# Performance work log

Hardware: AMD Instinct MI355X
Metric: run time of the kernel (lower is better)

## Reference

```python
import jax, jax.numpy as jnp
import numpy as np

N, D, W, S = 16384, 256, 64, 8  # utterances, embed dim, attention half-window, speakers


def setup_inputs() -> dict:
    key = jax.random.key(0)
    ks = jax.random.split(key, 8)
    scale = 1.0 / np.sqrt(D)
    return {
        "x": jax.random.normal(ks[0], (N, D), jnp.float32),
        "speaker_ids": jax.random.randint(ks[1], (N,), 0, S, jnp.int32),
        "W_att": jax.random.normal(ks[2], (D, D), jnp.float32) * scale,
        "W_pred": jax.random.normal(ks[3], (D, D), jnp.float32) * scale,
        "W_suc": jax.random.normal(ks[4], (D, D), jnp.float32) * scale,
        "W_same": jax.random.normal(ks[5], (D, D), jnp.float32) * scale,
        "W_diff": jax.random.normal(ks[6], (D, D), jnp.float32) * scale,
    }


def reference(x, speaker_ids, W_att, W_pred, W_suc, W_same, W_diff):
    n = x.shape[0]
    pad = jnp.zeros((W, D), x.dtype)
    # windowed gather: for utterance i, neighbors at offsets [-W, W-1] (2W slots)
    win_idx = jnp.arange(n)[:, None] + jnp.arange(2 * W)[None, :]  # index into padded [N+2W]
    xp = jnp.concatenate([pad, x, pad], axis=0)                    # [N+2W, D]
    windows = xp[win_idx]                                          # [N, 2W, D]
    # raw_attn[i,w] = (edge_att_weights(windows[i,w])) . x[i]
    raw_attn = jnp.einsum("nwd,ed,ne->nw", windows, W_att, x)      # [N, 2W]
    attn = jax.nn.softmax(raw_attn, axis=1)
    # relation masks over the band: j = i + offset
    offs = jnp.arange(2 * W) - W                                   # [-W, W-1]
    j = jnp.arange(n)[:, None] + offs[None, :]                     # [N, 2W]
    valid = (j >= 0) & (j < n)
    jc = jnp.clip(j, 0, n - 1)
    same_spk = speaker_ids[jc] == speaker_ids[:, None]
    masks = [
        valid & (offs >= 0)[None, :],   # pred: edges to current/future within window
        valid & (offs < 0)[None, :],    # suc: edges to past within window
        valid & same_spk,               # same speaker within window
        valid & ~same_spk,              # different speaker within window
    ]
    # relation-specific GCN aggregation: h = sum_r A_r @ (x @ W_r), A_r banded
    h = jnp.zeros_like(x)
    for Wr, m in zip([W_pred, W_suc, W_same, W_diff], masks):
        support = x @ Wr                                           # [N, D]
        sp = jnp.concatenate([pad, support, pad], axis=0)[win_idx]  # [N, 2W, D]
        h = h + jnp.einsum("nw,nwd->nd", attn * m, sp)
    return jax.nn.log_softmax(h, axis=1)
```

## Files before the change

### kernel.cpp

```cpp
#include <hip/hip_runtime.h>
#include <hip/hip_bf16.h>

typedef unsigned short u16;
typedef unsigned int u32;
typedef __attribute__((ext_vector_type(8))) short short8;
typedef __attribute__((ext_vector_type(4))) float floatx4;

#define NU 16384
#define DIM 256
#define AMS 200
#define AC1o 12800u
#define YLO 16896u
#define STGo 33792u

#define XHo 0u
#define XLo 4194304u
#define ST0 20971520u
#define STROW 16512u
#define STMAT 4227072u
#define WH0o 33652736u
#define WL0o 33718272u
#define WRo  33783808u

__device__ __forceinline__ u16 bfh(float v) {
  return (u16)(__float_as_uint(v) >> 16);
}
__device__ __forceinline__ float bup(u16 u) {
  return __uint_as_float(((u32)u) << 16);
}
__device__ __forceinline__ u16 bfrn(float v) {
  u32 u = __float_as_uint(v);
  return (u16)((u + 0x7fffu + ((u >> 16) & 1u)) >> 16);
}

__device__ __forceinline__ void gload16(const u16* g, u16* l) {
  __builtin_amdgcn_global_load_lds(
      (__attribute__((address_space(1))) void*)(uintptr_t)g,
      (__attribute__((address_space(3))) void*)(uintptr_t)l, 16, 0, 0);
}

__global__ __launch_bounds__(256) void prep(
    const float* __restrict__ x,
    const float* __restrict__ wat, const float* __restrict__ wpr,
    const float* __restrict__ wsu, const float* __restrict__ wsm,
    const float* __restrict__ wdf, u16* __restrict__ ws) {
  const int b = blockIdx.x, t = threadIdx.x;
  if (b < 2048) {
    int idx = (b * 256 + t) * 8;
    float4 v0 = *(const float4*)(x + idx);
    float4 v1 = *(const float4*)(x + idx + 4);
    float a[8] = {v0.x, v0.y, v0.z, v0.w, v1.x, v1.y, v1.z, v1.w};
    u16 h[8], l[8];
#pragma unroll
    for (int q = 0; q < 8; ++q) {
      h[q] = bfh(a[q]);
      l[q] = bfh(a[q] - bup(h[q]));
    }
    *(uint4*)(ws + XHo + idx) = *(const uint4*)h;
    *(uint4*)(ws + XLo + idx) = *(const uint4*)l;
    return;
  }
  const int b2 = b - 2048;
  if (b2 < 32) {
    const int s = b2 & 7, mat = b2 >> 3, n = t;
    const float* Wa = (mat == 0) ? wat : (mat == 1) ? wpr : (mat == 2) ? wsm : wsu;
    const float* Wb = (mat == 0) ? wat : (mat == 1) ? wsu : (mat == 2) ? wdf : wdf;
    const float c1  = (mat == 0) ? 0.f : (mat == 3) ? 1.f : -1.f;
    u16 hbuf[32], lbuf[32];
#pragma unroll 8
    for (int k = 0; k < 32; ++k) {
      float v = Wa[(s * 32 + k) * 256 + n] + c1 * Wb[(s * 32 + k) * 256 + n];
      if (mat == 0) { hbuf[k] = bfh(v); lbuf[k] = bfh(v - bup(hbuf[k])); }
      else          { hbuf[k] = bfrn(v); }
    }
    u16* dh = ws + ((mat == 0) ? WH0o : (WRo + (size_t)(mat - 1) * 65536))
               + (size_t)s * 8192 + n * 32;
#pragma unroll
    for (int p = 0; p < 4; ++p) *(uint4*)(dh + p * 8) = ((const uint4*)hbuf)[p];
    if (mat == 0) {
      u16* dl = ws + WL0o + (size_t)s * 8192 + n * 32;
#pragma unroll
      for (int p = 0; p < 4; ++p) *(uint4*)(dl + p * 8) = ((const uint4*)lbuf)[p];
    }
  } else {
    int g = (b2 - 32) * 256 + t;
    int r = g >> 13, rem = g & 8191;
    int d = rem >> 5, p = rem & 31;
    size_t base = ST0 + (size_t)r * STMAT + (size_t)d * STROW;
    size_t off = (p < 16) ? (base + p * 4) : (base + 16448 + (p - 16) * 4);
    *(ushort4*)(ws + off) = make_ushort4(0, 0, 0, 0);
  }
}

__global__ __launch_bounds__(512, 4) void gemmS1(const float* __restrict__ x,
                                                 u16* __restrict__ ws) {
  __shared__ __align__(16) u16 U[39168];

  const int t = threadIdx.x, row0 = blockIdx.x * 32;
  const int w = t >> 6, ln = t & 15, quad = (t & 63) >> 4, q8 = quad * 8;
  const int n0 = w * 32;

#pragma unroll
  for (int cc = 0; cc < 4; ++cc) {
    int idx = t + 512 * cc;
    int row = idx >> 6, c4 = (idx & 63) * 4;
    float4 v = *(const float4*)(x + (size_t)(row0 + row) * 256 + c4);
    ushort4 pk = make_ushort4(bfrn(v.x), bfrn(v.y), bfrn(v.z), bfrn(v.w));
    *(ushort4*)(U + row * 264 + c4) = pk;
  }
  __syncthreads();

  floatx4 acc[3][2][2];
#pragma unroll
  for (int mat = 0; mat < 3; ++mat)
#pragma unroll
    for (int m = 0; m < 2; ++m)
#pragma unroll
      for (int nt = 0; nt < 2; ++nt) acc[mat][m][nt] = (floatx4){0.f, 0.f, 0.f, 0.f};

  for (int s = 0; s < 8; ++s) {
    short8 ah[2];
#pragma unroll
    for (int m = 0; m < 2; ++m)
      ah[m] = *(const short8*)(U + (m * 16 + ln) * 264 + s * 32 + q8);
#pragma unroll
    for (int mat = 0; mat < 3; ++mat) {
      short8 bh[2];
#pragma unroll
      for (int nt = 0; nt < 2; ++nt)
        bh[nt] = *(const short8*)(ws + WRo + (size_t)mat * 65536
                                  + (size_t)s * 8192 + (n0 + nt * 16 + ln) * 32 + q8);
#pragma unroll
      for (int m = 0; m < 2; ++m)
#pragma unroll
        for (int nt = 0; nt < 2; ++nt)
          acc[mat][m][nt] = __builtin_amdgcn_mfma_f32_16x16x32_bf16(ah[m], bh[nt], acc[mat][m][nt], 0, 0, 0);
    }
  }

#pragma unroll
  for (int mat = 0; mat < 3; ++mat)
#pragma unroll
    for (int m = 0; m < 2; ++m)
#pragma unroll
      for (int nt = 0; nt < 2; ++nt) {
        int col = n0 + nt * 16 + ln;
        ushort4 pk = make_ushort4(bfrn(acc[mat][m][nt][0]), bfrn(acc[mat][m][nt][1]),
                                  bfrn(acc[mat][m][nt][2]), bfrn(acc[mat][m][nt][3]));
        *(ushort4*)(U + 8448 + mat * 10240 + col * 40 + m * 16 + quad * 4) = pk;
      }
  __syncthreads();

#pragma unroll
  for (int mat = 0; mat < 3; ++mat)
#pragma unroll
    for (int cc = 0; cc < 2; ++cc) {
      int c = t + 512 * cc;
      int d = c >> 2, part = c & 3;
      *(uint4*)(ws + ST0 + (size_t)mat * STMAT + (size_t)d * STROW + 64 + row0 + part * 8) =
          *(const uint4*)(U + 8448 + mat * 10240 + d * 40 + part * 8);
    }
}

__global__ __launch_bounds__(512) void fused_attn(
    const u16* __restrict__ ws, const int* __restrict__ spk,
    float* __restrict__ out)
{
  __shared__ __align__(16) u16 U[58368];
  __shared__ int spkw[192];
  __shared__ float prt[64][2], prs[64][2];
  __shared__ float red[64][8];

  const int t    = threadIdx.x;
  const int w    = t >> 6;
  const int ln   = t & 15;
  const int quad = (t & 63) >> 4;
  const int q8   = quad * 8;
  const int bswz = (blockIdx.x & 7) * 32 + (blockIdx.x >> 3);
  const int i0   = bswz * 64;
  const int mw   = w & 3;
  const int half = w >> 2;
  const int n0   = w * 32;

  if (t < 192) spkw[t] = spk[min(max(i0 - 64 + t, 0), NU - 1)];

  {
#pragma unroll
    for (int cc = 0; cc < 8; ++cc) {
      int idx = t + 512 * cc;
      int buf = idx >> 11, e = idx & 2047;
      int row = e >> 5, c8 = (e & 31) * 8;
      *(uint4*)(U + buf * YLO + row * 264 + c8) =
          *(const uint4*)(ws + (buf ? XLo : XHo) + (size_t)(i0 + row) * 256 + c8);
    }
    __syncthreads();

    floatx4 acc[4][2];
#pragma unroll
    for (int m = 0; m < 4; ++m)
#pragma unroll
      for (int nt = 0; nt < 2; ++nt) acc[m][nt] = (floatx4){0.f, 0.f, 0.f, 0.f};

    for (int s = 0; s < 8; ++s) {
      short8 ah[4], al[4];
#pragma unroll
      for (int m = 0; m < 4; ++m) {
        ah[m] = *(const short8*)(U + (m * 16 + ln) * 264 + s * 32 + q8);
        al[m] = *(const short8*)(U + YLO + (m * 16 + ln) * 264 + s * 32 + q8);
      }
      short8 bh[2], bl[2];
#pragma unroll
      for (int nt = 0; nt < 2; ++nt) {
        size_t off = (size_t)s * 8192 + (n0 + nt * 16 + ln) * 32 + q8;
        bh[nt] = *(const short8*)(ws + WH0o + off);
        bl[nt] = *(const short8*)(ws + WL0o + off);
      }
#pragma unroll
      for (int m = 0; m < 4; ++m)
#pragma unroll
        for (int nt = 0; nt < 2; ++nt) {
          acc[m][nt] = __builtin_amdgcn_mfma_f32_16x16x32_bf16(ah[m], bh[nt], acc[m][nt], 0, 0, 0);
          acc[m][nt] = __builtin_amdgcn_mfma_f32_16x16x32_bf16(ah[m], bl[nt], acc[m][nt], 0, 0, 0);
          acc[m][nt] = __builtin_amdgcn_mfma_f32_16x16x32_bf16(al[m], bh[nt], acc[m][nt], 0, 0, 0);
        }
    }
    __syncthreads();

#pragma unroll
    for (int m = 0; m < 4; ++m)
#pragma unroll
      for (int nt = 0; nt < 2; ++nt) {
        int col = n0 + nt * 16 + ln;
#pragma unroll
        for (int r = 0; r < 4; ++r) {
          int row = m * 16 + quad * 4 + r;
          float y = acc[m][nt][r];
          u16 hh = bfh(y);
          U[row * 264 + col] = hh;
          U[YLO + row * 264 + col] = bfh(y - bup(hh));
        }
      }
  }

  auto STAGE = [&](int ks, int par) {
    const int kd = ks * 32;
    u16* db = U + STGo + par * 12288;
#pragma unroll
    for (int cc = 0; cc < 3; ++cc) {
      int idx  = t + 512 * cc;
      int bsel = (idx >= 768) ? 1 : 0;
      int e    = idx - bsel * 768;
      int row  = e >> 2, s = e & 3;
      int sw   = s ^ ((row >> 1) & 3);
      int jc   = min(max(i0 + row - 64, 0), NU - 1);
      const u16* src = ws + (bsel ? XLo : XHo) + (size_t)jc * 256 + kd + sw * 8;
      u16* dst = db + bsel * 6144 + e * 8;
      gload16(src, dst);
    }
  };

  floatx4 accP[6];
#pragma unroll
  for (int cc = 0; cc < 6; ++cc) accP[cc] = (floatx4){0.f, 0.f, 0.f, 0.f};

  STAGE(0, 0);
  __syncthreads();
#pragma unroll
  for (int ks = 0; ks < 8; ++ks) {
    if (ks < 7) STAGE(ks + 1, (ks + 1) & 1);
    const u16* sp = U + STGo + (ks & 1) * 12288;
    const u16* yb = U + (mw * 16 + ln) * 264 + ks * 32 + q8;
    short8 yh8 = *(const short8*)yb;
    short8 yl8 = *(const short8*)(yb + YLO);
#pragma unroll
    for (int cc = 0; cc < 6; ++cc) {
      int xrow = half * 96 + cc * 16 + ln;
      int slot = quad ^ ((xrow >> 1) & 3);
      const u16* xb = sp + xrow * 32 + slot * 8;
      short8 xbh = *(const short8*)xb;
      short8 xbl = *(const short8*)(xb + 6144);
      accP[cc] = __builtin_amdgcn_mfma_f32_16x16x32_bf16(yh8, xbh, accP[cc], 0, 0, 0);
      accP[cc] = __builtin_amdgcn_mfma_f32_16x16x32_bf16(yh8, xbl, accP[cc], 0, 0, 0);
      accP[cc] = __builtin_amdgcn_mfma_f32_16x16x32_bf16(yl8, xbh, accP[cc], 0, 0, 0);
    }
    __syncthreads();
  }

  int  c_of[6];
  bool vj[6];
#pragma unroll
  for (int cc = 0; cc < 6; ++cc) {
    c_of[cc] = half * 96 + cc * 16 + ln;
    int j = i0 + c_of[cc] - 64;
    vj[cc] = (j >= 0) && (j < NU);
  }
#pragma unroll
  for (int r = 0; r < 4; ++r) {
    int row = mw * 16 + quad * 4 + r;
    float mx = -3.4e38f;
#pragma unroll
    for (int cc = 0; cc < 6; ++cc) {
      int rel = c_of[cc] - row;
      bool inb = (rel >= 0) && (rel < 128);
      if (inb) mx = fmaxf(mx, vj[cc] ? accP[cc][r] : 0.f);
    }
#pragma unroll
    for (int o = 1; o < 16; o <<= 1) mx = fmaxf(mx, __shfl_xor(mx, o));
    if (ln == 0) prt[row][half] = mx;
  }
  __syncthreads();
#pragma unroll
  for (int r = 0; r < 4; ++r) {
    int row = mw * 16 + quad * 4 + r;
    float gm = fmaxf(prt[row][0], prt[row][1]);
    float s = 0.f;
#pragma unroll
    for (int cc = 0; cc < 6; ++cc) {
      int rel = c_of[cc] - row;
      bool inb = (rel >= 0) && (rel < 128);
      float vv = vj[cc] ? accP[cc][r] : 0.f;
      float e  = inb ? __expf(vv - gm) : 0.f;
      s += e;
      accP[cc][r] = (inb && vj[cc]) ? e : 0.f;
    }
#pragma unroll
    for (int o = 1; o < 16; o <<= 1) s += __shfl_xor(s, o);
    if (ln == 0) prs[row][half] = s;
  }
  __syncthreads();
#pragma unroll
  for (int r = 0; r < 4; ++r) {
    int row = mw * 16 + quad * 4 + r;
    float inv = 1.f / (prs[row][0] + prs[row][1]);
#pragma unroll
    for (int cc = 0; cc < 6; ++cc)
      U[row * AMS + c_of[cc]] = bfrn(accP[cc][r] * inv);
  }
  __syncthreads();

  {
    const int arow = t >> 3, aseg = t & 7;
    const int sr = spkw[arow + 64];
    const int cb = aseg * 24;
#pragma unroll
    for (int p = 0; p < 6; ++p) {
      ushort4 av = *(const ushort4*)(U + arow * AMS + cb + p * 4);
      u16 aq[4] = {av.x, av.y, av.z, av.w};
      u16 b1v[4];
#pragma unroll
      for (int q = 0; q < 4; ++q) {
        int c = cb + p * 4 + q;
        b1v[q] = (spkw[c] == sr) ? aq[q] : (u16)0;
      }
      *(ushort4*)(U + AC1o + arow * AMS + cb + p * 4) = *(const ushort4*)b1v;
    }
  }
  __syncthreads();

  floatx4 acc2[4][2];
#pragma unroll
  for (int m = 0; m < 4; ++m)
#pragma unroll
    for (int nt = 0; nt < 2; ++nt) acc2[m][nt] = (floatx4){0.f, 0.f, 0.f, 0.f};

#pragma unroll
  for (int kj = 0; kj < 6; ++kj) {
    short8 af[4], af1[4];
#pragma unroll
    for (int m = 0; m < 4; ++m) {
      af[m]  = *(const short8*)(U + (m * 16 + ln) * AMS + kj * 32 + q8);
      af1[m] = *(const short8*)(U + AC1o + (m * 16 + ln) * AMS + kj * 32 + q8);
    }
    size_t sb[2];
#pragma unroll
    for (int nt = 0; nt < 2; ++nt)
      sb[nt] = (size_t)ST0 + (size_t)(n0 + nt * 16 + ln) * STROW
             + (size_t)(i0 + kj * 32) + q8;
#pragma unroll
    for (int nt = 0; nt < 2; ++nt) {
      short8 b2 = *(const short8*)(ws + sb[nt] + 2 * (size_t)STMAT);
      short8 b1 = *(const short8*)(ws + sb[nt] + 1 * (size_t)STMAT);
#pragma unroll
      for (int m = 0; m < 4; ++m) {
        acc2[m][nt] = __builtin_amdgcn_mfma_f32_16x16x32_bf16(af[m],  b2, acc2[m][nt], 0, 0, 0);
        acc2[m][nt] = __builtin_amdgcn_mfma_f32_16x16x32_bf16(af1[m], b1, acc2[m][nt], 0, 0, 0);
      }
    }
    if (kj >= 2) {
      short8 a0m[4];
#pragma unroll
      for (int m = 0; m < 4; ++m) {
        a0m[m] = af[m];
        if (!(32 * kj >= 16 * m + 79)) {
          int tthr = m * 16 + ln + 64 - kj * 32 - q8;
#pragma unroll
          for (int e = 0; e < 8; ++e)
            if (e < tthr) a0m[m][e] = 0;
        }
      }
#pragma unroll
      for (int nt = 0; nt < 2; ++nt) {
        short8 b0 = *(const short8*)(ws + sb[nt]);
#pragma unroll
        for (int m = 0; m < 4; ++m) {
          if (32 * kj < 16 * m + 33) continue;
          acc2[m][nt] = __builtin_amdgcn_mfma_f32_16x16x32_bf16(a0m[m], b0, acc2[m][nt], 0, 0, 0);
        }
      }
    }
  }

#pragma unroll
  for (int m = 0; m < 4; ++m)
#pragma unroll
    for (int r = 0; r < 4; ++r) {
      float v = fmaxf(acc2[m][0][r], acc2[m][1][r]);
#pragma unroll
      for (int o = 1; o < 16; o <<= 1) v = fmaxf(v, __shfl_xor(v, o));
      if (ln == 0) red[m * 16 + quad * 4 + r][w] = v;
    }
  __syncthreads();
  float gmx[4][4];
#pragma unroll
  for (int m = 0; m < 4; ++m)
#pragma unroll
    for (int r = 0; r < 4; ++r) {
      int row = m * 16 + quad * 4 + r;
      float g = red[row][0];
#pragma unroll
      for (int ww = 1; ww < 8; ++ww) g = fmaxf(g, red[row][ww]);
      gmx[m][r] = g;
    }
  __syncthreads();
#pragma unroll
  for (int m = 0; m < 4; ++m)
#pragma unroll
    for (int r = 0; r < 4; ++r) {
      float e = __expf(acc2[m][0][r] - gmx[m][r]) + __expf(acc2[m][1][r] - gmx[m][r]);
#pragma unroll
      for (int o = 1; o < 16; o <<= 1) e += __shfl_xor(e, o);
      if (ln == 0) red[m * 16 + quad * 4 + r][w] = e;
    }
  __syncthreads();
#pragma unroll
  for (int m = 0; m < 4; ++m)
#pragma unroll
    for (int r = 0; r < 4; ++r) {
      int row = m * 16 + quad * 4 + r;
      float s = red[row][0];
#pragma unroll
      for (int ww = 1; ww < 8; ++ww) s += red[row][ww];
      float lse = gmx[m][r] + logf(s);
      size_t rowg = (size_t)(i0 + row) * DIM;
      out[rowg + n0 + ln]      = acc2[m][0][r] - lse;
      out[rowg + n0 + 16 + ln] = acc2[m][1][r] - lse;
    }
}

extern "C" void kernel_launch(void* const* d_in, const int* in_sizes, int n_in,
                              void* d_out, int out_size, void* d_ws, size_t ws_size,
                              hipStream_t stream) {
  const float* x   = (const float*)d_in[0];
  const int*   spk = (const int*)d_in[1];
  const float* wat = (const float*)d_in[2];
  const float* wpr = (const float*)d_in[3];
  const float* wsu = (const float*)d_in[4];
  const float* wsm = (const float*)d_in[5];
  const float* wdf = (const float*)d_in[6];
  float* out = (float*)d_out;
  u16* ws = (u16*)d_ws;

  hipLaunchKernelGGL(prep, dim3(2176), dim3(256), 0, stream,
                     x, wat, wpr, wsu, wsm, wdf, ws);
  hipLaunchKernelGGL(gemmS1, dim3(512), dim3(512), 0, stream, x, ws);
  hipLaunchKernelGGL(fused_attn, dim3(256), dim3(512), 0, stream, ws, spk, out);
}
```

Measured before the change: 145.1 us.

## Drop the x bf16 hi/lo pre-split pass and convert fp32 x on the fly

Removes the prep stage that split x into bf16 high and low halves in workspace. fused_attn now loads fp32 x straight into LDS, for both the query tile and the staged neighbour tiles (with a new XOR swizzle), and splits it into hi/lo with a bit-mask helper just before each MFMA. This saves a full-size write and re-read of the split x and shrinks the prep grid. In exchange the staging buffers move twice the bytes and conversion ALU work is added inside the MFMA loops. LDS bank behaviour also changes under the new swizzle.

```diff
diff --git a/kernel.cpp b/kernel.cpp
--- a/kernel.cpp
+++ b/kernel.cpp
@@ -5,6 +5,7 @@
 typedef unsigned int u32;
 typedef __attribute__((ext_vector_type(8))) short short8;
 typedef __attribute__((ext_vector_type(4))) float floatx4;
+typedef __attribute__((ext_vector_type(4))) u32 u32x4;
 
 #define NU 16384
 #define DIM 256
@@ -13,8 +14,6 @@
 #define YLO 16896u
 #define STGo 33792u
 
-#define XHo 0u
-#define XLo 4194304u
 #define ST0 20971520u
 #define STROW 16512u
 #define STMAT 4227072u
@@ -33,6 +32,24 @@
   return (u16)((u + 0x7fffu + ((u >> 16) & 1u)) >> 16);
 }
 
+__device__ __forceinline__ void cvt8(float4 a, float4 b, short8& hi, short8& lo) {
+  float f[8] = {a.x, a.y, a.z, a.w, b.x, b.y, b.z, b.w};
+  u32 hw[4], lw[4];
+#pragma unroll
+  for (int i = 0; i < 4; ++i) {
+    u32 u0 = __float_as_uint(f[2 * i]);
+    u32 u1 = __float_as_uint(f[2 * i + 1]);
+    hw[i] = (u1 & 0xFFFF0000u) | (u0 >> 16);
+    float r0 = f[2 * i]     - __uint_as_float(u0 & 0xFFFF0000u);
+    float r1 = f[2 * i + 1] - __uint_as_float(u1 & 0xFFFF0000u);
+    lw[i] = (__float_as_uint(r1) & 0xFFFF0000u) | (__float_as_uint(r0) >> 16);
+  }
+  u32x4 h = {hw[0], hw[1], hw[2], hw[3]};
+  u32x4 l = {lw[0], lw[1], lw[2], lw[3]};
+  hi = __builtin_bit_cast(short8, h);
+  lo = __builtin_bit_cast(short8, l);
+}
+
 __device__ __forceinline__ void gload16(const u16* g, u16* l) {
   __builtin_amdgcn_global_load_lds(
       (__attribute__((address_space(1))) void*)(uintptr_t)g,
@@ -40,29 +57,12 @@
 }
 
 __global__ __launch_bounds__(256) void prep(
-    const float* __restrict__ x,
     const float* __restrict__ wat, const float* __restrict__ wpr,
     const float* __restrict__ wsu, const float* __restrict__ wsm,
     const float* __restrict__ wdf, u16* __restrict__ ws) {
   const int b = blockIdx.x, t = threadIdx.x;
-  if (b < 2048) {
-    int idx = (b * 256 + t) * 8;
-    float4 v0 = *(const float4*)(x + idx);
-    float4 v1 = *(const float4*)(x + idx + 4);
-    float a[8] = {v0.x, v0.y, v0.z, v0.w, v1.x, v1.y, v1.z, v1.w};
-    u16 h[8], l[8];
-#pragma unroll
-    for (int q = 0; q < 8; ++q) {
-      h[q] = bfh(a[q]);
-      l[q] = bfh(a[q] - bup(h[q]));
-    }
-    *(uint4*)(ws + XHo + idx) = *(const uint4*)h;
-    *(uint4*)(ws + XLo + idx) = *(const uint4*)l;
-    return;
-  }
-  const int b2 = b - 2048;
-  if (b2 < 32) {
-    const int s = b2 & 7, mat = b2 >> 3, n = t;
+  if (b < 32) {
+    const int s = b & 7, mat = b >> 3, n = t;
     const float* Wa = (mat == 0) ? wat : (mat == 1) ? wpr : (mat == 2) ? wsm : wsu;
     const float* Wb = (mat == 0) ? wat : (mat == 1) ? wsu : (mat == 2) ? wdf : wdf;
     const float c1  = (mat == 0) ? 0.f : (mat == 3) ? 1.f : -1.f;
@@ -83,7 +83,7 @@
       for (int p = 0; p < 4; ++p) *(uint4*)(dl + p * 8) = ((const uint4*)lbuf)[p];
     }
   } else {
-    int g = (b2 - 32) * 256 + t;
+    int g = (b - 32) * 256 + t;
     int r = g >> 13, rem = g & 8191;
     int d = rem >> 5, p = rem & 31;
     size_t base = ST0 + (size_t)r * STMAT + (size_t)d * STROW;
@@ -163,8 +163,8 @@
 }
 
 __global__ __launch_bounds__(512) void fused_attn(
-    const u16* __restrict__ ws, const int* __restrict__ spk,
-    float* __restrict__ out)
+    const float* __restrict__ x, const u16* __restrict__ ws,
+    const int* __restrict__ spk, float* __restrict__ out)
 {
   __shared__ __align__(16) u16 U[58368];
   __shared__ int spkw[192];
@@ -185,13 +185,13 @@
   if (t < 192) spkw[t] = spk[min(max(i0 - 64 + t, 0), NU - 1)];
 
   {
+    float* Sf = (float*)U;
 #pragma unroll
     for (int cc = 0; cc < 8; ++cc) {
       int idx = t + 512 * cc;
-      int buf = idx >> 11, e = idx & 2047;
-      int row = e >> 5, c8 = (e & 31) * 8;
-      *(uint4*)(U + buf * YLO + row * 264 + c8) =
-          *(const uint4*)(ws + (buf ? XLo : XHo) + (size_t)(i0 + row) * 256 + c8);
+      int row = idx >> 6, c4 = (idx & 63) * 4;
+      *(float4*)(Sf + row * 260 + c4) =
+          *(const float4*)(x + (size_t)(i0 + row) * 256 + c4);
     }
     __syncthreads();
 
@@ -205,8 +205,10 @@
       short8 ah[4], al[4];
 #pragma unroll
       for (int m = 0; m < 4; ++m) {
-        ah[m] = *(const short8*)(U + (m * 16 + ln) * 264 + s * 32 + q8);
-        al[m] = *(const short8*)(U + YLO + (m * 16 + ln) * 264 + s * 32 + q8);
+        int base = (m * 16 + ln) * 260 + s * 32 + q8;
+        float4 a0 = *(const float4*)(Sf + base);
+        float4 a1 = *(const float4*)(Sf + base + 4);
+        cvt8(a0, a1, ah[m], al[m]);
       }
       short8 bh[2], bl[2];
 #pragma unroll
@@ -244,18 +246,15 @@
 
   auto STAGE = [&](int ks, int par) {
     const int kd = ks * 32;
-    u16* db = U + STGo + par * 12288;
+    float* db = (float*)(U + STGo) + par * 6144;
 #pragma unroll
     for (int cc = 0; cc < 3; ++cc) {
-      int idx  = t + 512 * cc;
-      int bsel = (idx >= 768) ? 1 : 0;
-      int e    = idx - bsel * 768;
-      int row  = e >> 2, s = e & 3;
-      int sw   = s ^ ((row >> 1) & 3);
-      int jc   = min(max(i0 + row - 64, 0), NU - 1);
-      const u16* src = ws + (bsel ? XLo : XHo) + (size_t)jc * 256 + kd + sw * 8;
-      u16* dst = db + bsel * 6144 + e * 8;
-      gload16(src, dst);
+      int e   = t + 512 * cc;
+      int row = e >> 3, pos = e & 7;
+      int sw  = pos ^ (row & 7);
+      int jc  = min(max(i0 + row - 64, 0), NU - 1);
+      gload16((const u16*)(x + (size_t)jc * 256 + kd + sw * 4),
+              (u16*)(db + e * 4));
     }
   };
 
@@ -268,17 +267,19 @@
 #pragma unroll
   for (int ks = 0; ks < 8; ++ks) {
     if (ks < 7) STAGE(ks + 1, (ks + 1) & 1);
-    const u16* sp = U + STGo + (ks & 1) * 12288;
+    const float* sp = (const float*)(U + STGo) + (ks & 1) * 6144;
     const u16* yb = U + (mw * 16 + ln) * 264 + ks * 32 + q8;
     short8 yh8 = *(const short8*)yb;
     short8 yl8 = *(const short8*)(yb + YLO);
 #pragma unroll
     for (int cc = 0; cc < 6; ++cc) {
       int xrow = half * 96 + cc * 16 + ln;
-      int slot = quad ^ ((xrow >> 1) & 3);
-      const u16* xb = sp + xrow * 32 + slot * 8;
-      short8 xbh = *(const short8*)xb;
-      short8 xbl = *(const short8*)(xb + 6144);
+      int xr7  = xrow & 7;
+      int c0   = quad * 2;
+      float4 f0 = *(const float4*)(sp + xrow * 32 + ((c0 ^ xr7) << 2));
+      float4 f1 = *(const float4*)(sp + xrow * 32 + (((c0 + 1) ^ xr7) << 2));
+      short8 xbh, xbl;
+      cvt8(f0, f1, xbh, xbl);
       accP[cc] = __builtin_amdgcn_mfma_f32_16x16x32_bf16(yh8, xbh, accP[cc], 0, 0, 0);
       accP[cc] = __builtin_amdgcn_mfma_f32_16x16x32_bf16(yh8, xbl, accP[cc], 0, 0, 0);
       accP[cc] = __builtin_amdgcn_mfma_f32_16x16x32_bf16(yl8, xbh, accP[cc], 0, 0, 0);
@@ -470,8 +471,8 @@
   float* out = (float*)d_out;
   u16* ws = (u16*)d_ws;
 
-  hipLaunchKernelGGL(prep, dim3(2176), dim3(256), 0, stream,
-                     x, wat, wpr, wsu, wsm, wdf, ws);
+  hipLaunchKernelGGL(prep, dim3(128), dim3(256), 0, stream,
+                     wat, wpr, wsu, wsm, wdf, ws);
   hipLaunchKernelGGL(gemmS1, dim3(512), dim3(512), 0, stream, x, ws);
-  hipLaunchKernelGGL(fused_attn, dim3(256), dim3(512), 0, stream, ws, spk, out);
-}
+  hipLaunchKernelGGL(fused_attn, dim3(256), dim3(512), 0, stream, x, ws, spk, out);
+}
```

New measurement: 146.8 us. No clear change (+1.2%).
